# Optimization experiments

Hardware: AMD Instinct MI355X
Metric: run time of the kernel (lower is better)

## Reference

```python
import jax, jax.numpy as jnp
import numpy as np

B, T, I, H, L = 64, 1024, 256, 512, 2

def setup_inputs() -> dict:
    key = jax.random.key(0)
    ks = jax.random.split(key, 1 + 4 * L)
    inp = {"x": jax.random.normal(ks[0], (B, 1, I, T), dtype=jnp.float32)}
    s_in = 1.0 / np.sqrt(H)
    for l in range(L):
        in_dim = I if l == 0 else H
        k0, k1, k2, k3 = ks[1 + 4 * l: 5 + 4 * l]
        inp[f"W_ih{l}"] = jax.random.uniform(k0, (4 * H, in_dim), jnp.float32, -s_in, s_in)
        inp[f"W_hh{l}"] = jax.random.uniform(k1, (4 * H, H), jnp.float32, -s_in, s_in)
        inp[f"b_ih{l}"] = jax.random.uniform(k2, (4 * H,), jnp.float32, -s_in, s_in)
        inp[f"b_hh{l}"] = jax.random.uniform(k3, (4 * H,), jnp.float32, -s_in, s_in)
    return inp

def _lstm_layer(x, W_ih, W_hh, b_ih, b_hh):
    # x: [B, T, in_dim] -> outputs [B, T, H], (h_T, c_T) each [B, H]
    xp = jnp.einsum('bti,gi->btg', x, W_ih) + b_ih + b_hh  # [B, T, 4H]
    h0 = jnp.zeros((x.shape[0], H), x.dtype)
    c0 = jnp.zeros((x.shape[0], H), x.dtype)

    def step(carry, xt):
        h, c = carry
        gates = xt + h @ W_hh.T  # [B, 4H]
        i, f, g, o = jnp.split(gates, 4, axis=-1)  # PyTorch gate order: i,f,g,o
        i = jax.nn.sigmoid(i); f = jax.nn.sigmoid(f)
        g = jnp.tanh(g); o = jax.nn.sigmoid(o)
        c = f * c + i * g
        h = o * jnp.tanh(c)
        return (h, c), h

    (hT, cT), ys = jax.lax.scan(step, (h0, c0), jnp.swapaxes(xp, 0, 1))
    return jnp.swapaxes(ys, 0, 1), hT, cT

def reference(x, W_ih0, W_hh0, b_ih0, b_hh0, W_ih1, W_hh1, b_ih1, b_hh1):
    # x: [B, 1, I, T] -> squeeze(1), permute(0,2,1) -> [B, T, I]
    seq = jnp.transpose(jnp.squeeze(x, 1), (0, 2, 1))
    params = [(W_ih0, W_hh0, b_ih0, b_hh0), (W_ih1, W_hh1, b_ih1, b_hh1)]
    hs, cs = [], []
    out = seq
    for (W_ih, W_hh, b_ih, b_hh) in params:
        out, hT, cT = _lstm_layer(out, W_ih, W_hh, b_ih, b_hh)
        hs.append(hT); cs.append(cT)
    hidden = jnp.stack(hs, 0)  # [L, B, H]
    cell = jnp.stack(cs, 0)    # [L, B, H]
    return (out, (hidden, cell))
```

## Files before the change

kernel.cpp:

```cpp
#include <hip/hip_runtime.h>

#define HB 64
#define HT 1024
#define HI 256
#define HH 512

typedef short short8 __attribute__((ext_vector_type(8)));
typedef float f32x4 __attribute__((ext_vector_type(4)));

__device__ __forceinline__ unsigned short f2bf(float f) {
    unsigned u = __float_as_uint(f);
    u += 0x7FFF + ((u >> 16) & 1);
    return (unsigned short)(u >> 16);
}
__device__ __forceinline__ float bf2f(unsigned short s) {
    return __uint_as_float(((unsigned)s) << 16);
}
__device__ __forceinline__ float fsigmoid(float x) {
    return __builtin_amdgcn_rcpf(1.0f + __expf(-x));
}
__device__ __forceinline__ float ftanh(float x) {
    return 1.0f - 2.0f * __builtin_amdgcn_rcpf(__expf(2.0f * x) + 1.0f);
}

__device__ __forceinline__ short8 ld_frag(const unsigned long long* p) {
    union { unsigned long long u[2]; short8 s; } cv;
    cv.u[0] = __hip_atomic_load(p,     __ATOMIC_RELAXED, __HIP_MEMORY_SCOPE_AGENT);
    cv.u[1] = __hip_atomic_load(p + 1, __ATOMIC_RELAXED, __HIP_MEMORY_SCOPE_AGENT);
    return cv.s;
}

__global__ void pack_weights(const float* __restrict__ Wih0, const float* __restrict__ Whh0,
                             const float* __restrict__ bih0, const float* __restrict__ bhh0,
                             const float* __restrict__ Wih1, const float* __restrict__ Whh1,
                             const float* __restrict__ bih1, const float* __restrict__ bhh1,
                             unsigned short* __restrict__ wp0,
                             unsigned short* __restrict__ wp1,
                             float* __restrict__ bs) {
    int idx = blockIdx.x * 256 + threadIdx.x;
    int stride = gridDim.x * 256;
    const int NP0 = 128 * 24 * 512;
    const int NP1 = 128 * 32 * 512;
    for (int e = idx; e < NP0; e += stride) {
        int j = e & 7, l = (e >> 3) & 63, rem = e >> 9;
        int kt = rem % 24, nt = rem / 24;
        int n = nt * 16 + (l & 15);
        int k = kt * 32 + ((l >> 4) << 3) + j;
        float v = (k < HI) ? Wih0[n * HI + k] : Whh0[n * HH + (k - HI)];
        wp0[e] = f2bf(v);
    }
    for (int e = idx; e < NP1; e += stride) {
        int j = e & 7, l = (e >> 3) & 63, rem = e >> 9;
        int kt = rem & 31, nt = rem >> 5;
        int n = nt * 16 + (l & 15);
        int k = kt * 32 + ((l >> 4) << 3) + j;
        float v = (k < HH) ? Wih1[n * HH + k] : Whh1[n * HH + (k - HH)];
        wp1[e] = f2bf(v);
    }
    for (int e = idx; e < 2048; e += stride) {
        bs[e]        = bih0[e] + bhh0[e];
        bs[2048 + e] = bih1[e] + bhh1[e];
    }
}

__global__ void pack_x(const float* __restrict__ x, unsigned short* __restrict__ xp) {
    int tt = blockIdx.x;
    int ii = blockIdx.y;
    int bt = blockIdx.z;
    int w  = threadIdx.x;
    __shared__ unsigned short tile[512][16];
    int tloc = w & 15;
    for (int q = 0; q < 32; ++q) {
        int p = q * 16 + (w >> 4);
        int m = p >> 5, iloc = p & 31;
        int b = bt * 16 + m, i = ii * 32 + iloc, t = tt * 16 + tloc;
        tile[p][tloc] = f2bf(x[((size_t)b * HI + i) * HT + t]);
    }
    __syncthreads();
    int e  = w * 2;
    int l  = e >> 3, j0 = e & 7;
    int m  = l & 15;
    int i0 = ((l >> 4) << 3) + j0;
    for (int ti = 0; ti < 16; ++ti) {
        int t = tt * 16 + ti;
        size_t base = ((size_t)(t * 4 + bt) * 8 + ii) * 512;
        unsigned v0 = tile[m * 32 + i0][ti];
        unsigned v1 = tile[m * 32 + i0 + 1][ti];
        ((unsigned int*)xp)[(base + e) >> 1] = v0 | (v1 << 16);
    }
}

__global__ void init_flags(int* __restrict__ f, int n) {
    int idx = blockIdx.x * 256 + threadIdx.x;
    for (int e = idx; e < n; e += gridDim.x * 256) f[e] = 0;
}

__global__ void __launch_bounds__(256, 1) lstm_persist(
        const unsigned short* __restrict__ wp0,
        const unsigned short* __restrict__ wp1,
        const float* __restrict__ bs,
        const unsigned short* __restrict__ xp,
        unsigned long long* __restrict__ h0ring,
        unsigned long long* __restrict__ h1ring,
        int* __restrict__ flag0,
        int* __restrict__ flag1,
        float* __restrict__ out) {
    __shared__ int4 ldsw[8192];
    __shared__ unsigned long long stage[256];

    const int bid   = blockIdx.x;
    const int layer = bid >> 5;
    const int ut    = bid & 31;
    const int tid   = threadIdx.x;
    const int mt    = tid >> 6;
    const int l     = tid & 63;
    const int ul    = l & 15;
    const int q     = l >> 4;
    const int KT    = layer ? 32 : 24;

    const short8* ldsf = (const short8*)ldsw;
    unsigned short* stage_s = (unsigned short*)stage;

    {
        const unsigned short* wsrc = layer ? wp1 : wp0;
        for (int g = 0; g < 4; ++g) {
            const int4* src = (const int4*)(wsrc + (size_t)(g * 32 + ut) * KT * 512);
            int4* dst = ldsw + (size_t)g * KT * 64;
            for (int i = tid; i < KT * 64; i += 256) dst[i] = src[i];
        }
    }
    float bv[4];
    #pragma unroll
    for (int g = 0; g < 4; ++g) bv[g] = bs[layer * 2048 + g * HH + ut * 16 + ul];
    float cc[4] = {0.f, 0.f, 0.f, 0.f};
    __syncthreads();

    const int u = ut * 16 + ul;
    const int stg_w = mt * 256 + (ul >> 3) * 128 + (ul & 7);
    const size_t ring_dst_sub = (size_t)(tid >> 6) * 2048 +
                                (ut >> 1) * 128 + ((2 * ut) & 3) * 32 + (tid & 63);

    for (int t = 0; t < HT; ++t) {
        f32x4 acc[4];
        #pragma unroll
        for (int g = 0; g < 4; ++g) {
            f32x4 a; a[0] = bv[g]; a[1] = bv[g]; a[2] = bv[g]; a[3] = bv[g];
            acc[g] = a;
        }

        if (layer == 0) {
            const short8* xa = (const short8*)xp + ((size_t)t * 4 + mt) * 8 * 64;
            #pragma unroll
            for (int kt = 0; kt < 8; ++kt) {
                short8 a = xa[kt * 64 + l];
                #pragma unroll
                for (int g = 0; g < 4; ++g)
                    acc[g] = __builtin_amdgcn_mfma_f32_16x16x32_bf16(
                        a, ldsf[(g * 24 + kt) * 64 + l], acc[g], 0, 0, 0);
            }
            if (t > 0) {
                if (tid < 64) {
                    const int* p;
                    bool skip;
                    if (l < 32) { p = flag0 + (size_t)(t - 1) * 32 + l; skip = false; }
                    else        { p = flag1 + (size_t)(t >= 8 ? t - 8 : 0) * 32 + (l - 32);
                                  skip = (t < 8); }
                    for (;;) {
                        int v = skip ? 1 : __hip_atomic_load(p, __ATOMIC_RELAXED,
                                                             __HIP_MEMORY_SCOPE_AGENT);
                        if (__ballot(v != 0) == ~0ull) break;
                        __builtin_amdgcn_s_sleep(1);
                    }
                }
                __syncthreads();
                const unsigned long long* hb =
                    h0ring + ((size_t)(((t - 1) & 7) * 4 + mt)) * 2048;
                short8 af[16];
                #pragma unroll
                for (int kt = 0; kt < 16; ++kt) af[kt] = ld_frag(hb + kt * 128 + l * 2);
                #pragma unroll
                for (int kt = 0; kt < 16; ++kt) {
                    #pragma unroll
                    for (int g = 0; g < 4; ++g)
                        acc[g] = __builtin_amdgcn_mfma_f32_16x16x32_bf16(
                            af[kt], ldsf[(g * 24 + 8 + kt) * 64 + l], acc[g], 0, 0, 0);
                }
            }
        } else {
            if (tid < 64) {
                const int* p;
                bool skip;
                if (l < 32) { p = flag0 + (size_t)t * 32 + l; skip = false; }
                else        { p = flag1 + (size_t)(t > 0 ? t - 1 : 0) * 32 + (l - 32);
                              skip = (t == 0); }
                for (;;) {
                    int v = skip ? 1 : __hip_atomic_load(p, __ATOMIC_RELAXED,
                                                         __HIP_MEMORY_SCOPE_AGENT);
                    if (__ballot(v != 0) == ~0ull) break;
                    __builtin_amdgcn_s_sleep(1);
                }
            }
            __syncthreads();

            if (t > 0) {
                const unsigned long long* hb1 =
                    h1ring + ((size_t)(((t - 1) & 1) * 4 + mt)) * 2048;
                const unsigned long long* hb0 =
                    h0ring + ((size_t)((t & 7) * 4 + mt)) * 2048;
                short8 af1[16];
                short8 af0[16];
                #pragma unroll
                for (int kt = 0; kt < 16; ++kt) af1[kt] = ld_frag(hb1 + kt * 128 + l * 2);
                #pragma unroll
                for (int kt = 0; kt < 16; ++kt) af0[kt] = ld_frag(hb0 + kt * 128 + l * 2);
                #pragma unroll
                for (int kt = 0; kt < 16; ++kt) {
                    #pragma unroll
                    for (int g = 0; g < 4; ++g)
                        acc[g] = __builtin_amdgcn_mfma_f32_16x16x32_bf16(
                            af1[kt], ldsf[(g * 32 + 16 + kt) * 64 + l], acc[g], 0, 0, 0);
                }
                #pragma unroll
                for (int kt = 0; kt < 16; ++kt) {
                    #pragma unroll
                    for (int g = 0; g < 4; ++g)
                        acc[g] = __builtin_amdgcn_mfma_f32_16x16x32_bf16(
                            af0[kt], ldsf[(g * 32 + kt) * 64 + l], acc[g], 0, 0, 0);
                }
            } else {
                const unsigned long long* hb0 =
                    h0ring + ((size_t)((t & 7) * 4 + mt)) * 2048;
                short8 af0[16];
                #pragma unroll
                for (int kt = 0; kt < 16; ++kt) af0[kt] = ld_frag(hb0 + kt * 128 + l * 2);
                #pragma unroll
                for (int kt = 0; kt < 16; ++kt) {
                    #pragma unroll
                    for (int g = 0; g < 4; ++g)
                        acc[g] = __builtin_amdgcn_mfma_f32_16x16x32_bf16(
                            af0[kt], ldsf[(g * 32 + kt) * 64 + l], acc[g], 0, 0, 0);
                }
            }
        }

        #pragma unroll
        for (int r = 0; r < 4; ++r) {
            int m = q * 4 + r;
            int b = mt * 16 + m;
            float iv = fsigmoid(acc[0][r]);
            float fv = fsigmoid(acc[1][r]);
            float gv = ftanh(acc[2][r]);
            float ov = fsigmoid(acc[3][r]);
            float c = fv * cc[r] + iv * gv;
            cc[r] = c;
            float h = ov * ftanh(c);
            stage_s[stg_w + m * 8] = f2bf(h);
            if (t == HT - 1) {
                out[33554432 + layer * 32768 + b * 512 + u] = h;
                out[33619968 + layer * 32768 + b * 512 + u] = c;
            }
        }
        __syncthreads();

        {
            unsigned long long v = stage[tid];
            unsigned long long* ring = layer ? h1ring : h0ring;
            int slot = layer ? (t & 1) : (t & 7);
            __hip_atomic_store(ring + (size_t)slot * 8192 + ring_dst_sub, v,
                               __ATOMIC_RELAXED, __HIP_MEMORY_SCOPE_AGENT);
        }

        asm volatile("s_waitcnt vmcnt(0)" ::: "memory");
        __syncthreads();
        if (tid == 0) {
            int* fl = layer ? flag1 : flag0;
            __hip_atomic_store(fl + (size_t)t * 32 + ut, 1,
                               __ATOMIC_RELAXED, __HIP_MEMORY_SCOPE_AGENT);
        }

        if (layer == 1) {
            int b = tid >> 2, ch = tid & 3;
            const unsigned short* sp = stage_s + (b >> 4) * 256 + (ch >> 1) * 128 +
                                       (b & 15) * 8 + (ch & 1) * 4;
            f32x4 o;
            o[0] = bf2f(sp[0]); o[1] = bf2f(sp[1]);
            o[2] = bf2f(sp[2]); o[3] = bf2f(sp[3]);
            *(f32x4*)&out[((size_t)b * HT + t) * HH + ut * 16 + ch * 4] = o;
        }
    }
}

extern "C" void kernel_launch(void* const* d_in, const int* in_sizes, int n_in,
                              void* d_out, int out_size, void* d_ws, size_t ws_size,
                              hipStream_t stream) {
    const float* x    = (const float*)d_in[0];
    const float* Wih0 = (const float*)d_in[1];
    const float* Whh0 = (const float*)d_in[2];
    const float* bih0 = (const float*)d_in[3];
    const float* bhh0 = (const float*)d_in[4];
    const float* Wih1 = (const float*)d_in[5];
    const float* Whh1 = (const float*)d_in[6];
    const float* bih1 = (const float*)d_in[7];
    const float* bhh1 = (const float*)d_in[8];

    char* ws = (char*)d_ws;
    unsigned short* wp0 = (unsigned short*)(ws + 0);
    unsigned short* wp1 = (unsigned short*)(ws + 3145728);
    float*          bsv = (float*)(ws + 7340032);
    unsigned short* xp  = (unsigned short*)(ws + 7356416);
    int*   flag0        = (int*)(ws + 40910848);
    int*   flag1        = (int*)(ws + 41041920);
    unsigned long long* h0r = (unsigned long long*)(ws + 41172992);
    unsigned long long* h1r = (unsigned long long*)(ws + 41697280);
    float* out = (float*)d_out;

    pack_weights<<<2048, 256, 0, stream>>>(Wih0, Whh0, bih0, bhh0,
                                           Wih1, Whh1, bih1, bhh1, wp0, wp1, bsv);
    pack_x<<<dim3(64, 8, 4), 256, 0, stream>>>(x, xp);
    init_flags<<<64, 256, 0, stream>>>(flag0, 65536);

    lstm_persist<<<64, 256, 0, stream>>>(wp0, wp1, bsv, xp, h0r, h1r,
                                         flag0, flag1, out);
}
```

Baseline: 8.787 ms.

## Embed timestep tags in h ring entries to replace per-step flag handshakes

Each hidden-state ring entry now carries its timestep tag next to the data, written with a single 16-byte system-coherent store. Consumers poll the data directly until every tag matches the expected step, so the layer-0 flag array, the flag wait with its block-wide barriers and the post-store barrier are gone. Layer 0 shrinks its ring to 4 slots and only checks layer 1's flag (four steps back) for backpressure, prefetching that flag early. The intent is to cut per-step synchronisation latency on the recurrent critical path, at the cost of doubled ring traffic from padding and repeated full-fragment reloads while spinning.

```diff
diff --git a/kernel.cpp b/kernel.cpp
--- a/kernel.cpp
+++ b/kernel.cpp
@@ -7,6 +7,7 @@
 
 typedef short short8 __attribute__((ext_vector_type(8)));
 typedef float f32x4 __attribute__((ext_vector_type(4)));
+typedef int   i32x4 __attribute__((ext_vector_type(4)));
 
 __device__ __forceinline__ unsigned short f2bf(float f) {
     unsigned u = __float_as_uint(f);
@@ -23,11 +24,45 @@
     return 1.0f - 2.0f * __builtin_amdgcn_rcpf(__expf(2.0f * x) + 1.0f);
 }
 
-__device__ __forceinline__ short8 ld_frag(const unsigned long long* p) {
-    union { unsigned long long u[2]; short8 s; } cv;
-    cv.u[0] = __hip_atomic_load(p,     __ATOMIC_RELAXED, __HIP_MEMORY_SCOPE_AGENT);
-    cv.u[1] = __hip_atomic_load(p + 1, __ATOMIC_RELAXED, __HIP_MEMORY_SCOPE_AGENT);
-    return cv.s;
+__device__ __forceinline__ void st_pair16(void* p, i32x4 v) {
+    asm volatile("global_store_dwordx4 %0, %1, off sc0 sc1"
+                 :: "v"(p), "v"(v) : "memory");
+}
+
+__device__ __forceinline__ void pull16(const char* base0, int expect, short8* af) {
+    for (;;) {
+        i32x4 v[32];
+        const char* b = base0;
+        #pragma unroll
+        for (int bi = 0; bi < 8; ++bi) {
+            asm volatile("global_load_dwordx4 %0, %1, off sc0 sc1"
+                         : "=v"(v[bi * 4 + 0]) : "v"(b));
+            asm volatile("global_load_dwordx4 %0, %1, off offset:16 sc0 sc1"
+                         : "=v"(v[bi * 4 + 1]) : "v"(b));
+            asm volatile("global_load_dwordx4 %0, %1, off offset:2048 sc0 sc1"
+                         : "=v"(v[bi * 4 + 2]) : "v"(b));
+            asm volatile("global_load_dwordx4 %0, %1, off offset:2064 sc0 sc1"
+                         : "=v"(v[bi * 4 + 3]) : "v"(b));
+            b += 4096;
+        }
+        asm volatile("s_waitcnt vmcnt(0)" ::: "memory");
+        __builtin_amdgcn_sched_barrier(0);
+        int ok = 1;
+        #pragma unroll
+        for (int i = 0; i < 32; ++i)
+            ok &= (v[i][2] == expect) & (v[i][3] == 0);
+        if (__ballot(ok != 0) == ~0ull) {
+            #pragma unroll
+            for (int kt = 0; kt < 16; ++kt) {
+                union { int i4[4]; short8 s; } u;
+                u.i4[0] = v[2 * kt][0];     u.i4[1] = v[2 * kt][1];
+                u.i4[2] = v[2 * kt + 1][0]; u.i4[3] = v[2 * kt + 1][1];
+                af[kt] = u.s;
+            }
+            return;
+        }
+        __builtin_amdgcn_s_sleep(2);
+    }
 }
 
 __global__ void pack_weights(const float* __restrict__ Wih0, const float* __restrict__ Whh0,
@@ -90,9 +125,14 @@
     }
 }
 
-__global__ void init_flags(int* __restrict__ f, int n) {
+__global__ void init_sync(int* __restrict__ flag1,
+                          int4* __restrict__ h0r, int4* __restrict__ h1r) {
     int idx = blockIdx.x * 256 + threadIdx.x;
-    for (int e = idx; e < n; e += gridDim.x * 256) f[e] = 0;
+    int stride = gridDim.x * 256;
+    for (int e = idx; e < 32768; e += stride) flag1[e] = 0;
+    int4 s; s.x = 0; s.y = 0; s.z = -1; s.w = -1;
+    for (int e = idx; e < 32768; e += stride) h0r[e] = s;
+    for (int e = idx; e < 16384; e += stride) h1r[e] = s;
 }
 
 __global__ void __launch_bounds__(256, 1) lstm_persist(
@@ -100,9 +140,8 @@
         const unsigned short* __restrict__ wp1,
         const float* __restrict__ bs,
         const unsigned short* __restrict__ xp,
-        unsigned long long* __restrict__ h0ring,
-        unsigned long long* __restrict__ h1ring,
-        int* __restrict__ flag0,
+        char* __restrict__ h0ring,
+        char* __restrict__ h1ring,
         int* __restrict__ flag1,
         float* __restrict__ out) {
     __shared__ int4 ldsw[8192];
@@ -137,8 +176,7 @@
 
     const int u = ut * 16 + ul;
     const int stg_w = mt * 256 + (ul >> 3) * 128 + (ul & 7);
-    const size_t ring_dst_sub = (size_t)(tid >> 6) * 2048 +
-                                (ut >> 1) * 128 + ((2 * ut) & 3) * 32 + (tid & 63);
+    const int ring_sub = (ut >> 1) * 128 + ((2 * ut) & 3) * 32 + (tid & 63);
 
     for (int t = 0; t < HT; ++t) {
         f32x4 acc[4];
@@ -149,6 +187,11 @@
         }
 
         if (layer == 0) {
+            int fv = 1;
+            if (t >= 4 && l < 32)
+                fv = __hip_atomic_load(flag1 + (size_t)(t - 4) * 32 + l,
+                                       __ATOMIC_RELAXED, __HIP_MEMORY_SCOPE_AGENT);
+
             const short8* xa = (const short8*)xp + ((size_t)t * 4 + mt) * 8 * 64;
             #pragma unroll
             for (int kt = 0; kt < 8; ++kt) {
@@ -159,25 +202,10 @@
                         a, ldsf[(g * 24 + kt) * 64 + l], acc[g], 0, 0, 0);
             }
             if (t > 0) {
-                if (tid < 64) {
-                    const int* p;
-                    bool skip;
-                    if (l < 32) { p = flag0 + (size_t)(t - 1) * 32 + l; skip = false; }
-                    else        { p = flag1 + (size_t)(t >= 8 ? t - 8 : 0) * 32 + (l - 32);
-                                  skip = (t < 8); }
-                    for (;;) {
-                        int v = skip ? 1 : __hip_atomic_load(p, __ATOMIC_RELAXED,
-                                                             __HIP_MEMORY_SCOPE_AGENT);
-                        if (__ballot(v != 0) == ~0ull) break;
-                        __builtin_amdgcn_s_sleep(1);
-                    }
-                }
-                __syncthreads();
-                const unsigned long long* hb =
-                    h0ring + ((size_t)(((t - 1) & 7) * 4 + mt)) * 2048;
+                const char* hb = h0ring +
+                    (size_t)((((t - 1) & 3) * 4 + mt)) * 32768 + (size_t)l * 32;
                 short8 af[16];
-                #pragma unroll
-                for (int kt = 0; kt < 16; ++kt) af[kt] = ld_frag(hb + kt * 128 + l * 2);
+                pull16(hb, t - 1, af);
                 #pragma unroll
                 for (int kt = 0; kt < 16; ++kt) {
                     #pragma unroll
@@ -186,33 +214,51 @@
                             af[kt], ldsf[(g * 24 + 8 + kt) * 64 + l], acc[g], 0, 0, 0);
                 }
             }
+
+            #pragma unroll
+            for (int r = 0; r < 4; ++r) {
+                int m = q * 4 + r;
+                int b = mt * 16 + m;
+                float iv = fsigmoid(acc[0][r]);
+                float fv2 = fsigmoid(acc[1][r]);
+                float gv = ftanh(acc[2][r]);
+                float ov = fsigmoid(acc[3][r]);
+                float c = fv2 * cc[r] + iv * gv;
+                cc[r] = c;
+                float h = ov * ftanh(c);
+                stage_s[stg_w + m * 8] = f2bf(h);
+                if (t == HT - 1) {
+                    out[33554432 + b * 512 + u] = h;
+                    out[33619968 + b * 512 + u] = c;
+                }
+            }
+
+            if (t >= 4) {
+                if (__ballot(fv != 0) != ~0ull) {
+                    const int* p = flag1 + (size_t)(t - 4) * 32 + (l & 31);
+                    while (__ballot((l >= 32) ||
+                           (__hip_atomic_load(p, __ATOMIC_RELAXED,
+                                              __HIP_MEMORY_SCOPE_AGENT) != 0)) != ~0ull)
+                        __builtin_amdgcn_s_sleep(1);
+                }
+            }
+
+            {
+                unsigned long long v = stage[tid];
+                i32x4 pv;
+                pv[0] = (int)(unsigned)(v & 0xffffffffull);
+                pv[1] = (int)(unsigned)(v >> 32);
+                pv[2] = t; pv[3] = 0;
+                char* dst = h0ring +
+                    ((size_t)((t & 3) * 4 + mt) * 2048 + ring_sub) * 16;
+                st_pair16(dst, pv);
+            }
         } else {
-            if (tid < 64) {
-                const int* p;
-                bool skip;
-                if (l < 32) { p = flag0 + (size_t)t * 32 + l; skip = false; }
-                else        { p = flag1 + (size_t)(t > 0 ? t - 1 : 0) * 32 + (l - 32);
-                              skip = (t == 0); }
-                for (;;) {
-                    int v = skip ? 1 : __hip_atomic_load(p, __ATOMIC_RELAXED,
-                                                         __HIP_MEMORY_SCOPE_AGENT);
-                    if (__ballot(v != 0) == ~0ull) break;
-                    __builtin_amdgcn_s_sleep(1);
-                }
-            }
-            __syncthreads();
-
             if (t > 0) {
-                const unsigned long long* hb1 =
-                    h1ring + ((size_t)(((t - 1) & 1) * 4 + mt)) * 2048;
-                const unsigned long long* hb0 =
-                    h0ring + ((size_t)((t & 7) * 4 + mt)) * 2048;
+                const char* hb1 = h1ring +
+                    (size_t)((((t - 1) & 1) * 4 + mt)) * 32768 + (size_t)l * 32;
                 short8 af1[16];
-                short8 af0[16];
-                #pragma unroll
-                for (int kt = 0; kt < 16; ++kt) af1[kt] = ld_frag(hb1 + kt * 128 + l * 2);
-                #pragma unroll
-                for (int kt = 0; kt < 16; ++kt) af0[kt] = ld_frag(hb0 + kt * 128 + l * 2);
+                pull16(hb1, t - 1, af1);
                 #pragma unroll
                 for (int kt = 0; kt < 16; ++kt) {
                     #pragma unroll
@@ -220,6 +266,12 @@
                         acc[g] = __builtin_amdgcn_mfma_f32_16x16x32_bf16(
                             af1[kt], ldsf[(g * 32 + 16 + kt) * 64 + l], acc[g], 0, 0, 0);
                 }
+            }
+            {
+                const char* hb0 = h0ring +
+                    (size_t)(((t & 3) * 4 + mt)) * 32768 + (size_t)l * 32;
+                short8 af0[16];
+                pull16(hb0, t, af0);
                 #pragma unroll
                 for (int kt = 0; kt < 16; ++kt) {
                     #pragma unroll
@@ -227,65 +279,51 @@
                         acc[g] = __builtin_amdgcn_mfma_f32_16x16x32_bf16(
                             af0[kt], ldsf[(g * 32 + kt) * 64 + l], acc[g], 0, 0, 0);
                 }
-            } else {
-                const unsigned long long* hb0 =
-                    h0ring + ((size_t)((t & 7) * 4 + mt)) * 2048;
-                short8 af0[16];
-                #pragma unroll
-                for (int kt = 0; kt < 16; ++kt) af0[kt] = ld_frag(hb0 + kt * 128 + l * 2);
-                #pragma unroll
-                for (int kt = 0; kt < 16; ++kt) {
-                    #pragma unroll
-                    for (int g = 0; g < 4; ++g)
-                        acc[g] = __builtin_amdgcn_mfma_f32_16x16x32_bf16(
-                            af0[kt], ldsf[(g * 32 + kt) * 64 + l], acc[g], 0, 0, 0);
-                }
-            }
-        }
-
-        #pragma unroll
-        for (int r = 0; r < 4; ++r) {
-            int m = q * 4 + r;
-            int b = mt * 16 + m;
-            float iv = fsigmoid(acc[0][r]);
-            float fv = fsigmoid(acc[1][r]);
-            float gv = ftanh(acc[2][r]);
-            float ov = fsigmoid(acc[3][r]);
-            float c = fv * cc[r] + iv * gv;
-            cc[r] = c;
-            float h = ov * ftanh(c);
-            stage_s[stg_w + m * 8] = f2bf(h);
-            if (t == HT - 1) {
-                out[33554432 + layer * 32768 + b * 512 + u] = h;
-                out[33619968 + layer * 32768 + b * 512 + u] = c;
-            }
-        }
-        __syncthreads();
-
-        {
-            unsigned long long v = stage[tid];
-            unsigned long long* ring = layer ? h1ring : h0ring;
-            int slot = layer ? (t & 1) : (t & 7);
-            __hip_atomic_store(ring + (size_t)slot * 8192 + ring_dst_sub, v,
-                               __ATOMIC_RELAXED, __HIP_MEMORY_SCOPE_AGENT);
-        }
-
-        asm volatile("s_waitcnt vmcnt(0)" ::: "memory");
-        __syncthreads();
-        if (tid == 0) {
-            int* fl = layer ? flag1 : flag0;
-            __hip_atomic_store(fl + (size_t)t * 32 + ut, 1,
-                               __ATOMIC_RELAXED, __HIP_MEMORY_SCOPE_AGENT);
-        }
-
-        if (layer == 1) {
-            int b = tid >> 2, ch = tid & 3;
-            const unsigned short* sp = stage_s + (b >> 4) * 256 + (ch >> 1) * 128 +
-                                       (b & 15) * 8 + (ch & 1) * 4;
-            f32x4 o;
-            o[0] = bf2f(sp[0]); o[1] = bf2f(sp[1]);
-            o[2] = bf2f(sp[2]); o[3] = bf2f(sp[3]);
-            *(f32x4*)&out[((size_t)b * HT + t) * HH + ut * 16 + ch * 4] = o;
+            }
+
+            #pragma unroll
+            for (int r = 0; r < 4; ++r) {
+                int m = q * 4 + r;
+                int b = mt * 16 + m;
+                float iv = fsigmoid(acc[0][r]);
+                float fv2 = fsigmoid(acc[1][r]);
+                float gv = ftanh(acc[2][r]);
+                float ov = fsigmoid(acc[3][r]);
+                float c = fv2 * cc[r] + iv * gv;
+                cc[r] = c;
+                float h = ov * ftanh(c);
+                stage_s[stg_w + m * 8] = f2bf(h);
+                if (t == HT - 1) {
+                    out[33554432 + 32768 + b * 512 + u] = h;
+                    out[33619968 + 32768 + b * 512 + u] = c;
+                }
+            }
+
+            {
+                unsigned long long v = stage[tid];
+                i32x4 pv;
+                pv[0] = (int)(unsigned)(v & 0xffffffffull);
+                pv[1] = (int)(unsigned)(v >> 32);
+                pv[2] = t; pv[3] = 0;
+                char* dst = h1ring +
+                    ((size_t)((t & 1) * 4 + mt) * 2048 + ring_sub) * 16;
+                st_pair16(dst, pv);
+            }
+
+            __syncthreads();
+            if (tid == 0)
+                __hip_atomic_store(flag1 + (size_t)t * 32 + ut, 1,
+                                   __ATOMIC_RELAXED, __HIP_MEMORY_SCOPE_AGENT);
+
+            {
+                int b = tid >> 2, ch = tid & 3;
+                const unsigned short* sp = stage_s + (b >> 4) * 256 + (ch >> 1) * 128 +
+                                           (b & 15) * 8 + (ch & 1) * 4;
+                f32x4 o;
+                o[0] = bf2f(sp[0]); o[1] = bf2f(sp[1]);
+                o[2] = bf2f(sp[2]); o[3] = bf2f(sp[3]);
+                *(f32x4*)&out[((size_t)b * HT + t) * HH + ut * 16 + ch * 4] = o;
+            }
         }
     }
 }
@@ -308,17 +346,16 @@
     unsigned short* wp1 = (unsigned short*)(ws + 3145728);
     float*          bsv = (float*)(ws + 7340032);
     unsigned short* xp  = (unsigned short*)(ws + 7356416);
-    int*   flag0        = (int*)(ws + 40910848);
-    int*   flag1        = (int*)(ws + 41041920);
-    unsigned long long* h0r = (unsigned long long*)(ws + 41172992);
-    unsigned long long* h1r = (unsigned long long*)(ws + 41697280);
+    int*   flag1        = (int*)(ws + 40910848);
+    char*  h0r          = (char*)(ws + 41041920);
+    char*  h1r          = (char*)(ws + 41566208);
     float* out = (float*)d_out;
 
     pack_weights<<<2048, 256, 0, stream>>>(Wih0, Whh0, bih0, bhh0,
                                            Wih1, Whh1, bih1, bhh1, wp0, wp1, bsv);
     pack_x<<<dim3(64, 8, 4), 256, 0, stream>>>(x, xp);
-    init_flags<<<64, 256, 0, stream>>>(flag0, 65536);
+    init_sync<<<64, 256, 0, stream>>>(flag1, (int4*)h0r, (int4*)h1r);
 
     lstm_persist<<<64, 256, 0, stream>>>(wp0, wp1, bsv, xp, h0r, h1r,
-                                         flag0, flag1, out);
-}
+                                         flag1, out);
+}
```

After: 12.39 ms. 1.41x slower.
